# Optimization experiments

Measured on AMD Instinct MI355X. Metric: run time of the kernel, lower is better.

## Reference

```python
import jax, jax.numpy as jnp
import numpy as np

B, N, P = 8192, 4096, 8
D = N // P  # 512
EPS = 1e-5


def setup_inputs() -> dict:
    key = jax.random.key(0)
    ks = jax.random.split(key, 7)
    bound = 1.0 / np.sqrt(D)
    return {
        "x": jax.random.normal(ks[0], (B, N), dtype=jnp.float32),
        "weights1": jax.random.normal(ks[1], (P, D, D), dtype=jnp.float32) * bound,
        "bias1": jax.random.uniform(ks[2], (N,), jnp.float32, -bound, bound),
        "weights2": jax.random.normal(ks[3], (P, D, D), dtype=jnp.float32) * bound,
        "bias2": jax.random.uniform(ks[4], (N,), jnp.float32, -bound, bound),
        "bn_weight": jnp.ones((N,), jnp.float32),
        "bn_bias": jnp.zeros((N,), jnp.float32),
        "gamma3": jax.random.normal(ks[5], (N,), jnp.float32) * 0.1,
        "beta3": jax.random.normal(ks[6], (N,), jnp.float32) * 0.1,
    }


def _block_matmul(x, w):
    # x: [B, N], w: [P, D, D] -> equivalent to x @ block_diag(*w)
    b = x.shape[0]
    return jnp.einsum("bpd,pde->bpe", x.reshape(b, P, D), w).reshape(b, N)


def reference(x, weights1, bias1, weights2, bias2, bn_weight, bn_bias, gamma3, beta3):
    h = _block_matmul(x, weights1) + bias1  # [B, N]
    # BatchNorm1d in training mode: biased batch statistics over the batch axis
    mean = jnp.mean(h, axis=0)
    var = jnp.mean((h - mean) ** 2, axis=0)
    o1 = (h - mean) * jax.lax.rsqrt(var + EPS) * bn_weight + bn_bias
    o3 = _block_matmul(o1, weights2) + bias2 + x  # residual
    # sigmoid-gated activation: (gamma + sigmoid(beta*x)*(1-gamma)) * x
    o4 = (gamma3 + jax.nn.sigmoid(beta3 * o3) * (1.0 - gamma3)) * o3
    return o4
```

## Files before the change

### kernel.cpp

```cpp
#include <hip/hip_runtime.h>
#include <hip/hip_bf16.h>
#include <cstdint>
#include <cstddef>

#define B_ROWS 8192
#define N_COLS 4096
#define P_BLK 8
#define D_BLK 512
#define EPSV 1e-5f

typedef __bf16 bf16x8 __attribute__((ext_vector_type(8)));
typedef float f32x4 __attribute__((ext_vector_type(4)));

__device__ __forceinline__ void async_ld16(const void* g, void* l) {
    __builtin_amdgcn_global_load_lds(
        (const __attribute__((address_space(1))) void*)g,
        (__attribute__((address_space(3))) void*)l,
        16, 0, 0);
}

__device__ __forceinline__ void decode_tile(int n, int& row_base, int& col_base) {
    const int row_tile = n >> 5;
    const int col_tile = ((n & 7) << 2) | ((n >> 3) & 3);
    row_base = row_tile * 128;
    col_base = col_tile * 128;
}

__global__ __launch_bounds__(256) void cvt_x_k(const float* __restrict__ x,
                                               __hip_bfloat16* __restrict__ xb) {
    size_t i = ((size_t)blockIdx.x * 256 + threadIdx.x) * 8;
    float4 v0 = *(const float4*)(x + i);
    float4 v1 = *(const float4*)(x + i + 4);
    union { __hip_bfloat16 h[8]; uint4 u; } r;
    r.h[0] = __float2bfloat16(v0.x); r.h[1] = __float2bfloat16(v0.y);
    r.h[2] = __float2bfloat16(v0.z); r.h[3] = __float2bfloat16(v0.w);
    r.h[4] = __float2bfloat16(v1.x); r.h[5] = __float2bfloat16(v1.y);
    r.h[6] = __float2bfloat16(v1.z); r.h[7] = __float2bfloat16(v1.w);
    *(uint4*)(xb + i) = r.u;
}

__global__ __launch_bounds__(256) void tr_w_k(const float* __restrict__ W,
                                              const float* __restrict__ scale,
                                              __hip_bfloat16* __restrict__ Wt) {
    __shared__ float t[32][33];
    int p = blockIdx.z;
    int d0 = blockIdx.x * 32, e0 = blockIdx.y * 32;
    const float* Wp = W + (size_t)p * D_BLK * D_BLK;
    for (int j = 0; j < 32; j += 8) {
        int d = d0 + threadIdx.y + j;
        float v = Wp[(size_t)d * D_BLK + e0 + threadIdx.x];
        if (scale) v *= scale[p * D_BLK + d];
        t[threadIdx.y + j][threadIdx.x] = v;
    }
    __syncthreads();
    __hip_bfloat16* Wtp = Wt + (size_t)p * D_BLK * D_BLK;
    for (int j = 0; j < 32; j += 8) {
        int e = e0 + threadIdx.y + j;
        Wtp[(size_t)e * D_BLK + d0 + threadIdx.x] =
            __float2bfloat16(t[threadIdx.x][threadIdx.y + j]);
    }
}

__global__ __launch_bounds__(256) void finalize_k(const float* __restrict__ sum,
                                                  const float* __restrict__ sumsq,
                                                  const float* __restrict__ bnw,
                                                  const float* __restrict__ bnb,
                                                  float* __restrict__ a,
                                                  float* __restrict__ c) {
    int i = blockIdx.x * 256 + threadIdx.x;
    float m = sum[i] * (1.0f / B_ROWS);
    float var = sumsq[i] * (1.0f / B_ROWS) - m * m;
    float ai = bnw[i] * rsqrtf(var + EPSV);
    a[i] = ai;
    c[i] = bnb[i] - m * ai;
}

__global__ __launch_bounds__(256) void bias2p_k(const float* __restrict__ W2,
                                                const float* __restrict__ c,
                                                const float* __restrict__ bias2,
                                                float* __restrict__ out) {
    int col = blockIdx.x * 256 + threadIdx.x;
    int p = col >> 9;
    int e = col & (D_BLK - 1);
    const float* Wp = W2 + (size_t)p * D_BLK * D_BLK + e;
    const float* cp = c + p * D_BLK;
    float acc = 0.0f;
    for (int d = 0; d < D_BLK; d++) acc += cp[d] * Wp[(size_t)d * D_BLK];
    out[col] = bias2[col] + acc;
}

__device__ __forceinline__ void gemm_core(const __hip_bfloat16* __restrict__ A,
                                          const __hip_bfloat16* __restrict__ Bt,
                                          int row_base, int col_base,
                                          f32x4 acc[4][4]) {
    __shared__ __hip_bfloat16 As[128 * 32];
    __shared__ __hip_bfloat16 Bs[128 * 32];

    const int tid = threadIdx.x;
    const int lane = tid & 63;
    const int wave = tid >> 6;
    const int wm = (wave >> 1) * 64;
    const int wn = (wave & 1) * 64;
    const int p = col_base >> 9;
    const int ebase = col_base & (D_BLK - 1);

    const int ar = tid >> 2;
    const int c4 = tid & 3;
    const int kq8 = (c4 ^ ((tid >> 3) & 3)) * 8;
    const int dst_off = ar * 32 + c4 * 8;

    const __hip_bfloat16* a_src0 = A + (size_t)(row_base + ar) * N_COLS + p * D_BLK + kq8;
    const __hip_bfloat16* a_src1 = a_src0 + (size_t)64 * N_COLS;
    const __hip_bfloat16* b_src0 = Bt + (size_t)(p * D_BLK + ebase + ar) * D_BLK + kq8;
    const __hip_bfloat16* b_src1 = b_src0 + (size_t)64 * D_BLK;
    __hip_bfloat16* a_dst0 = &As[dst_off];
    __hip_bfloat16* a_dst1 = &As[dst_off + 64 * 32];
    __hip_bfloat16* b_dst0 = &Bs[dst_off];
    __hip_bfloat16* b_dst1 = &Bs[dst_off + 64 * 32];

    const int fm = lane & 15;
    const int fkoff = ((lane >> 4) ^ ((fm >> 1) & 3)) * 8;

    for (int i = 0; i < 4; i++)
        for (int j = 0; j < 4; j++)
            acc[i][j] = (f32x4){0.0f, 0.0f, 0.0f, 0.0f};

    for (int k0 = 0; k0 < D_BLK; k0 += 32) {
        async_ld16(a_src0, a_dst0);
        async_ld16(a_src1, a_dst1);
        async_ld16(b_src0, b_dst0);
        async_ld16(b_src1, b_dst1);
        a_src0 += 32; a_src1 += 32; b_src0 += 32; b_src1 += 32;
        __syncthreads();

        bf16x8 af[4], bfr[4];
#pragma unroll
        for (int i = 0; i < 4; i++)
            af[i] = *(const bf16x8*)&As[(wm + i * 16 + fm) * 32 + fkoff];
#pragma unroll
        for (int j = 0; j < 4; j++)
            bfr[j] = *(const bf16x8*)&Bs[(wn + j * 16 + fm) * 32 + fkoff];
#pragma unroll
        for (int i = 0; i < 4; i++)
#pragma unroll
            for (int j = 0; j < 4; j++)
                acc[i][j] = __builtin_amdgcn_mfma_f32_16x16x32_bf16(
                    af[i], bfr[j], acc[i][j], 0, 0, 0);
        __syncthreads();
    }
}

__global__ __launch_bounds__(256) void gemm1_k(const __hip_bfloat16* __restrict__ xb,
                                               const __hip_bfloat16* __restrict__ w1t,
                                               const float* __restrict__ bias1,
                                               __hip_bfloat16* __restrict__ h,
                                               float* __restrict__ sum,
                                               float* __restrict__ sumsq) {
    int row_base, col_base;
    decode_tile(blockIdx.x, row_base, col_base);

    f32x4 acc[4][4];
    gemm_core(xb, w1t, row_base, col_base, acc);

    const int tid = threadIdx.x;
    const int lane = tid & 63;
    const int wave = tid >> 6;
    const int wm = (wave >> 1) * 64;
    const int wn = (wave & 1) * 64;
    const int cr = (lane >> 4) * 4;
    const int cc = lane & 15;

#pragma unroll
    for (int j = 0; j < 4; j++) {
        const int col = col_base + wn + j * 16 + cc;
        const float b1 = bias1[col];
        float s = 0.0f, sq = 0.0f;
#pragma unroll
        for (int i = 0; i < 4; i++) {
            const int row0 = row_base + wm + i * 16 + cr;
#pragma unroll
            for (int r = 0; r < 4; r++) {
                float v = acc[i][j][r] + b1;
                h[(size_t)(row0 + r) * N_COLS + col] = __float2bfloat16(v);
                s += v;
                sq += v * v;
            }
        }
        s  += __shfl_xor(s, 16);  s  += __shfl_xor(s, 32);
        sq += __shfl_xor(sq, 16); sq += __shfl_xor(sq, 32);
        if (lane < 16) {
            atomicAdd(&sum[col], s);
            atomicAdd(&sumsq[col], sq);
        }
    }
}

__global__ __launch_bounds__(256) void gemm2_k(const __hip_bfloat16* __restrict__ h,
                                               const __hip_bfloat16* __restrict__ w2t,
                                               const float* __restrict__ bias2p,
                                               const __hip_bfloat16* __restrict__ xb,
                                               const float* __restrict__ gamma3,
                                               const float* __restrict__ beta3,
                                               float* __restrict__ out) {
    int row_base, col_base;
    decode_tile(blockIdx.x, row_base, col_base);

    f32x4 acc[4][4];
    gemm_core(h, w2t, row_base, col_base, acc);

    const int tid = threadIdx.x;
    const int lane = tid & 63;
    const int wave = tid >> 6;
    const int wm = (wave >> 1) * 64;
    const int wn = (wave & 1) * 64;
    const int cr = (lane >> 4) * 4;
    const int cc = lane & 15;

#pragma unroll
    for (int j = 0; j < 4; j++) {
        const int col = col_base + wn + j * 16 + cc;
        const float bb = bias2p[col];
        const float g  = gamma3[col];
        const float be = beta3[col];
#pragma unroll
        for (int i = 0; i < 4; i++) {
            const int row0 = row_base + wm + i * 16 + cr;
#pragma unroll
            for (int r = 0; r < 4; r++) {
                const size_t idx = (size_t)(row0 + r) * N_COLS + col;
                float o3 = acc[i][j][r] + bb + __bfloat162float(xb[idx]);
                float sg = 1.0f / (1.0f + expf(-be * o3));
                out[idx] = (g + sg * (1.0f - g)) * o3;
            }
        }
    }
}

extern "C" void kernel_launch(void* const* d_in, const int* in_sizes, int n_in,
                              void* d_out, int out_size, void* d_ws, size_t ws_size,
                              hipStream_t stream) {
    const float* x     = (const float*)d_in[0];
    const float* W1    = (const float*)d_in[1];
    const float* bias1 = (const float*)d_in[2];
    const float* W2    = (const float*)d_in[3];
    const float* bias2 = (const float*)d_in[4];
    const float* bnw   = (const float*)d_in[5];
    const float* bnb   = (const float*)d_in[6];
    const float* gam3  = (const float*)d_in[7];
    const float* bet3  = (const float*)d_in[8];
    float* out = (float*)d_out;

    char* ws = (char*)d_ws;
    const size_t XB_BYTES = (size_t)B_ROWS * N_COLS * 2;
    const size_t H_BYTES  = (size_t)B_ROWS * N_COLS * 2;
    const size_t WT_BYTES = (size_t)P_BLK * D_BLK * D_BLK * 2;
    const size_t V_BYTES  = (size_t)N_COLS * 4;

    __hip_bfloat16* xb   = (__hip_bfloat16*)(ws);
    __hip_bfloat16* hbuf = (__hip_bfloat16*)(ws + XB_BYTES);
    __hip_bfloat16* w1t  = (__hip_bfloat16*)(ws + XB_BYTES + H_BYTES);
    __hip_bfloat16* w2t  = (__hip_bfloat16*)(ws + XB_BYTES + H_BYTES + WT_BYTES);
    float* sums  = (float*)(ws + XB_BYTES + H_BYTES + 2 * WT_BYTES);
    float* sumsq = (float*)((char*)sums + V_BYTES);
    float* a_sc  = (float*)((char*)sums + 2 * V_BYTES);
    float* c_sh  = (float*)((char*)sums + 3 * V_BYTES);
    float* b2p   = (float*)((char*)sums + 4 * V_BYTES);

    (void)in_sizes; (void)n_in; (void)out_size; (void)ws_size;

    hipMemsetAsync(sums, 0, 2 * V_BYTES, stream);

    cvt_x_k<<<dim3((B_ROWS * N_COLS) / (256 * 8)), dim3(256), 0, stream>>>(x, xb);
    tr_w_k<<<dim3(16, 16, 8), dim3(32, 8), 0, stream>>>(W1, nullptr, w1t);
    gemm1_k<<<dim3((B_ROWS / 128) * (N_COLS / 128)), dim3(256), 0, stream>>>(
        xb, w1t, bias1, hbuf, sums, sumsq);
    finalize_k<<<dim3(N_COLS / 256), dim3(256), 0, stream>>>(sums, sumsq, bnw, bnb, a_sc, c_sh);
    tr_w_k<<<dim3(16, 16, 8), dim3(32, 8), 0, stream>>>(W2, a_sc, w2t);
    bias2p_k<<<dim3(N_COLS / 256), dim3(256), 0, stream>>>(W2, c_sh, bias2, b2p);
    gemm2_k<<<dim3((B_ROWS / 128) * (N_COLS / 128)), dim3(256), 0, stream>>>(
        hbuf, w2t, b2p, xb, gam3, bet3, out);
}
```

Before: 403.3 us.

## Double-buffer GEMM LDS tiles, split bias2p reduction, use fast sigmoid

```diff
diff --git a/kernel.cpp b/kernel.cpp
--- a/kernel.cpp
+++ b/kernel.cpp
@@ -82,19 +82,20 @@
     int col = blockIdx.x * 256 + threadIdx.x;
     int p = col >> 9;
     int e = col & (D_BLK - 1);
-    const float* Wp = W2 + (size_t)p * D_BLK * D_BLK + e;
-    const float* cp = c + p * D_BLK;
-    float acc = 0.0f;
-    for (int d = 0; d < D_BLK; d++) acc += cp[d] * Wp[(size_t)d * D_BLK];
-    out[col] = bias2[col] + acc;
+    int d0 = blockIdx.y * (D_BLK / 8);
+    const float* Wp = W2 + (size_t)p * D_BLK * D_BLK + (size_t)d0 * D_BLK + e;
+    const float* cp = c + p * D_BLK + d0;
+    float acc = (blockIdx.y == 0) ? bias2[col] : 0.0f;
+    for (int d = 0; d < D_BLK / 8; d++) acc += cp[d] * Wp[(size_t)d * D_BLK];
+    atomicAdd(&out[col], acc);
 }
 
 __device__ __forceinline__ void gemm_core(const __hip_bfloat16* __restrict__ A,
                                           const __hip_bfloat16* __restrict__ Bt,
                                           int row_base, int col_base,
                                           f32x4 acc[4][4]) {
-    __shared__ __hip_bfloat16 As[128 * 32];
-    __shared__ __hip_bfloat16 Bs[128 * 32];
+    __shared__ __hip_bfloat16 As[2][128 * 32];
+    __shared__ __hip_bfloat16 Bs[2][128 * 32];
 
     const int tid = threadIdx.x;
     const int lane = tid & 63;
@@ -113,10 +114,6 @@
     const __hip_bfloat16* a_src1 = a_src0 + (size_t)64 * N_COLS;
     const __hip_bfloat16* b_src0 = Bt + (size_t)(p * D_BLK + ebase + ar) * D_BLK + kq8;
     const __hip_bfloat16* b_src1 = b_src0 + (size_t)64 * D_BLK;
-    __hip_bfloat16* a_dst0 = &As[dst_off];
-    __hip_bfloat16* a_dst1 = &As[dst_off + 64 * 32];
-    __hip_bfloat16* b_dst0 = &Bs[dst_off];
-    __hip_bfloat16* b_dst1 = &Bs[dst_off + 64 * 32];
 
     const int fm = lane & 15;
     const int fkoff = ((lane >> 4) ^ ((fm >> 1) & 3)) * 8;
@@ -125,28 +122,49 @@
         for (int j = 0; j < 4; j++)
             acc[i][j] = (f32x4){0.0f, 0.0f, 0.0f, 0.0f};
 
+    async_ld16(a_src0, &As[0][dst_off]);
+    async_ld16(a_src1, &As[0][dst_off + 64 * 32]);
+    async_ld16(b_src0, &Bs[0][dst_off]);
+    async_ld16(b_src1, &Bs[0][dst_off + 64 * 32]);
+
+    int cur = 0;
     for (int k0 = 0; k0 < D_BLK; k0 += 32) {
-        async_ld16(a_src0, a_dst0);
-        async_ld16(a_src1, a_dst1);
-        async_ld16(b_src0, b_dst0);
-        async_ld16(b_src1, b_dst1);
-        a_src0 += 32; a_src1 += 32; b_src0 += 32; b_src1 += 32;
-        __syncthreads();
+        if (k0 + 32 < D_BLK) {
+            __hip_bfloat16* ad = &As[cur ^ 1][dst_off];
+            __hip_bfloat16* bd = &Bs[cur ^ 1][dst_off];
+            async_ld16(a_src0 + 32, ad);
+            async_ld16(a_src1 + 32, ad + 64 * 32);
+            async_ld16(b_src0 + 32, bd);
+            async_ld16(b_src1 + 32, bd + 64 * 32);
+            a_src0 += 32; a_src1 += 32; b_src0 += 32; b_src1 += 32;
+            asm volatile("s_waitcnt vmcnt(4)" ::: "memory");
+        } else {
+            asm volatile("s_waitcnt vmcnt(0)" ::: "memory");
+        }
+        __builtin_amdgcn_s_barrier();
+        asm volatile("" ::: "memory");
 
         bf16x8 af[4], bfr[4];
+        const __hip_bfloat16* Asc = &As[cur][0];
+        const __hip_bfloat16* Bsc = &Bs[cur][0];
 #pragma unroll
         for (int i = 0; i < 4; i++)
-            af[i] = *(const bf16x8*)&As[(wm + i * 16 + fm) * 32 + fkoff];
+            af[i] = *(const bf16x8*)&Asc[(wm + i * 16 + fm) * 32 + fkoff];
 #pragma unroll
         for (int j = 0; j < 4; j++)
-            bfr[j] = *(const bf16x8*)&Bs[(wn + j * 16 + fm) * 32 + fkoff];
+            bfr[j] = *(const bf16x8*)&Bsc[(wn + j * 16 + fm) * 32 + fkoff];
+        asm volatile("s_waitcnt lgkmcnt(0)" ::: "memory");
+        __builtin_amdgcn_sched_barrier(0);
+        __builtin_amdgcn_s_barrier();
+        asm volatile("" ::: "memory");
+
 #pragma unroll
         for (int i = 0; i < 4; i++)
 #pragma unroll
             for (int j = 0; j < 4; j++)
                 acc[i][j] = __builtin_amdgcn_mfma_f32_16x16x32_bf16(
                     af[i], bfr[j], acc[i][j], 0, 0, 0);
-        __syncthreads();
+        cur ^= 1;
     }
 }
 
@@ -229,7 +247,7 @@
             for (int r = 0; r < 4; r++) {
                 const size_t idx = (size_t)(row0 + r) * N_COLS + col;
                 float o3 = acc[i][j][r] + bb + __bfloat162float(xb[idx]);
-                float sg = 1.0f / (1.0f + expf(-be * o3));
+                float sg = __fdividef(1.0f, 1.0f + __expf(-be * o3));
                 out[idx] = (g + sg * (1.0f - g)) * o3;
             }
         }
@@ -261,14 +279,14 @@
     __hip_bfloat16* w1t  = (__hip_bfloat16*)(ws + XB_BYTES + H_BYTES);
     __hip_bfloat16* w2t  = (__hip_bfloat16*)(ws + XB_BYTES + H_BYTES + WT_BYTES);
     float* sums  = (float*)(ws + XB_BYTES + H_BYTES + 2 * WT_BYTES);
-    float* sumsq = (float*)((char*)sums + V_BYTES);
-    float* a_sc  = (float*)((char*)sums + 2 * V_BYTES);
-    float* c_sh  = (float*)((char*)sums + 3 * V_BYTES);
-    float* b2p   = (float*)((char*)sums + 4 * V_BYTES);
+    float* sumsq = sums + N_COLS;
+    float* b2p   = sums + 2 * N_COLS;
+    float* a_sc  = sums + 3 * N_COLS;
+    float* c_sh  = sums + 4 * N_COLS;
 
     (void)in_sizes; (void)n_in; (void)out_size; (void)ws_size;
 
-    hipMemsetAsync(sums, 0, 2 * V_BYTES, stream);
+    hipMemsetAsync(sums, 0, 3 * V_BYTES, stream);
 
     cvt_x_k<<<dim3((B_ROWS * N_COLS) / (256 * 8)), dim3(256), 0, stream>>>(x, xb);
     tr_w_k<<<dim3(16, 16, 8), dim3(32, 8), 0, stream>>>(W1, nullptr, w1t);
@@ -276,7 +294,7 @@
         xb, w1t, bias1, hbuf, sums, sumsq);
     finalize_k<<<dim3(N_COLS / 256), dim3(256), 0, stream>>>(sums, sumsq, bnw, bnb, a_sc, c_sh);
     tr_w_k<<<dim3(16, 16, 8), dim3(32, 8), 0, stream>>>(W2, a_sc, w2t);
-    bias2p_k<<<dim3(N_COLS / 256), dim3(256), 0, stream>>>(W2, c_sh, bias2, b2p);
+    bias2p_k<<<dim3(N_COLS / 256, 8), dim3(256), 0, stream>>>(W2, c_sh, bias2, b2p);
     gemm2_k<<<dim3((B_ROWS / 128) * (N_COLS / 128)), dim3(256), 0, stream>>>(
         hbuf, w2t, b2p, xb, gam3, bet3, out);
 }
```

After: 390.5 us. 1.03x faster.
